# Kernel tuning notes

Measured on AMD Instinct MI355X. Metric: run time of the kernel, lower is better.

The kernel has to match this reference:

```python
import jax, jax.numpy as jnp
import numpy as np

# Model dims (from CerebroOriginal defaults)
B, C, T, E, H, NB, NC = 256, 14, 8, 180, 5, 6, 4
DH = E // H          # 36
S = C * T            # 112 tokens
MLP = 4 * E          # 720


def qdq(x):
    """Int8 per-tensor fake quant-dequant (Brevitas Int8ActPerTensorFloat-style), STE."""
    s = jnp.maximum(jnp.max(jnp.abs(x)) / 127.0, 1e-8)
    y = jnp.clip(jnp.round(x / s), -128.0, 127.0) * s
    return x + jax.lax.stop_gradient(y - x)


def ln(x, g, b):
    m = jnp.mean(x, axis=-1, keepdims=True)
    v = jnp.var(x, axis=-1, keepdims=True)
    return (x - m) * jax.lax.rsqrt(v + 1e-5) * g + b


def qlinear(x, w, b):
    """QuantLinear: int8 input quant + int8 per-tensor weight quant, float bias."""
    return qdq(x) @ qdq(w).T + b


def setup_inputs() -> dict:
    key = jax.random.key(0)
    ks = jax.random.split(key, 16)
    r = lambda k, sh: (0.05 * jax.random.normal(k, sh)).astype(jnp.float32)
    f32 = jnp.float32
    return {
        "x": jax.random.normal(ks[0], (B, C, T), dtype=f32),
        "proj_w": r(ks[1], (E, C)), "proj_b": jnp.zeros((E,), f32),
        "ln1_g": jnp.ones((NB, E), f32), "ln1_b": jnp.zeros((NB, E), f32),
        "wq": r(ks[2], (NB, E, E)), "bq": jnp.zeros((NB, E), f32),
        "wk": r(ks[3], (NB, E, E)), "bk": jnp.zeros((NB, E), f32),
        "wv": r(ks[4], (NB, E, E)), "bv": jnp.zeros((NB, E), f32),
        "wo": r(ks[5], (NB, E, E)), "bo": jnp.zeros((NB, E), f32),
        "ln2_g": jnp.ones((NB, E), f32), "ln2_b": jnp.zeros((NB, E), f32),
        "fc1_w": r(ks[6], (NB, MLP, E)), "fc1_b": jnp.zeros((NB, MLP), f32),
        "fc2_w": r(ks[7], (NB, E, MLP)), "fc2_b": jnp.zeros((NB, E), f32),
        "fn_g": jnp.ones((E,), f32), "fn_b": jnp.zeros((E,), f32),
        "cls_w": r(ks[8], (NC, E)), "cls_b": jnp.zeros((NC,), f32),
    }


def forward(x, proj_w, proj_b, ln1_g, ln1_b, wq, bq, wk, bk, wv, bv, wo, bo,
            ln2_g, ln2_b, fc1_w, fc1_b, fc2_w, fc2_b, fn_g, fn_b, cls_w, cls_b):
    # input quant -> [B,T,C] -> proj -> [B,T,E]
    h = jnp.transpose(qdq(x), (0, 2, 1))
    h = qlinear(h, proj_w, proj_b)
    # expand over channels then flatten to [B, C*T, E] (channel-major token layout)
    h = jnp.broadcast_to(h[:, None], (B, C, T, E)).reshape(B, S, E)

    for i in range(NB):
        # --- attention sub-block ---
        r1 = h
        a = qdq(ln(h, ln1_g[i], ln1_b[i])).reshape(B, C, T, E)
        if i % 2 == 0:  # temporal attention: attend over T within each channel
            a = a.reshape(B * C, T, E)
            L = T
        else:           # channel attention: attend over C within each time step
            a = jnp.transpose(a, (0, 2, 1, 3)).reshape(B * T, C, E)
            L = C
        q = qlinear(a, wq[i], bq[i]).reshape(-1, L, H, DH)
        k = qlinear(a, wk[i], bk[i]).reshape(-1, L, H, DH)
        v = qlinear(a, wv[i], bv[i]).reshape(-1, L, H, DH)
        scores = jnp.einsum('nlhd,nmhd->nhlm', q, k) / jnp.sqrt(jnp.float32(DH))
        att = jax.nn.softmax(scores, axis=-1)
        o = jnp.einsum('nhlm,nmhd->nlhd', att, v).reshape(-1, L, E)
        o = qlinear(o, wo[i], bo[i])
        if i % 2 == 0:
            o = o.reshape(B, C, T, E)
        else:
            o = jnp.transpose(o.reshape(B, T, C, E), (0, 2, 1, 3))
        h = r1 + o.reshape(B, S, E)

        # --- MLP sub-block ---
        r2 = h
        m = qdq(ln(h, ln2_g[i], ln2_b[i]))
        m = qlinear(m, fc1_w[i], fc1_b[i])
        m = qdq(jax.nn.gelu(m))
        m = qlinear(m, fc2_w[i], fc2_b[i])
        h = r2 + m

    h = qdq(ln(h, fn_g, fn_b))
    pooled = jnp.mean(h, axis=1)                 # QuantMean over tokens -> [B, E]
    return qlinear(pooled, cls_w, cls_b)         # [B, NC]


def reference(x, proj_w, proj_b, ln1_g, ln1_b, wq, bq, wk, bk, wv, bv, wo, bo,
              ln2_g, ln2_b, fc1_w, fc1_b, fc2_w, fc2_b, fn_g, fn_b, cls_w, cls_b):
    return forward(x, proj_w, proj_b, ln1_g, ln1_b, wq, bq, wk, bk, wv, bv, wo, bo,
                   ln2_g, ln2_b, fc1_w, fc1_b, fc2_w, fc2_b, fn_g, fn_b, cls_w, cls_b)
```

## Files before the change

### kernel.cpp

```cpp
#include <hip/hip_runtime.h>
#include <math.h>

#define E 180
#define S 112
#define Bb 256
#define CC 14
#define TT 8
#define HH 5
#define DH 36
#define NBLK 6
#define MLPD 720
#define M_TOK (Bb*S)
#define BUF ((size_t)M_TOK * E)

#define KP1 192
#define KP2 736

#define WQ8_OFF   0
#define WK8_OFF   36864
#define WV8_OFF   73728
#define WO8_OFF   110592
#define FC18_OFF  147456
#define FC28_OFF  285696
#define WBLK      427008

#define SLOT_X    0
#define SLOT_PW   1
#define SLOT_CW   2
#define SLOT_POOL 3
#define SLOT_FLN  4
#define SLOT_WQ   8
#define SLOT_WK   16
#define SLOT_WV   24
#define SLOT_WO   32
#define SLOT_FC1  40
#define SLOT_FC2  48
#define SLOT_LN1  56
#define SLOT_O    64
#define SLOT_LN2  72
#define SLOT_GELU 80
#define SLOT_GXMAX 88
#define SLOT_GXA   96
#define SLOT_GXB   104
#define SLOT_GDIR  112

#define XL (-0.7535)
#define XR (-0.7515)

typedef unsigned long long ull;
typedef __attribute__((ext_vector_type(8))) short short8;
typedef __attribute__((ext_vector_type(4))) float f32x4;

__device__ __forceinline__ double slot_scale(const ull* s){
  return fmax(__longlong_as_double((long long)*s) / 127.0, 1e-8);
}
__device__ __forceinline__ void atomic_max_d(ull* p, double v){
  atomicMax(p, (ull)__double_as_longlong(v));
}
__device__ __forceinline__ ull enc_d(double d){
  ull b = (ull)__double_as_longlong(d);
  return (b >> 63) ? ~b : (b | 0x8000000000000000ULL);
}
__device__ __forceinline__ double dec_d(ull k){
  ull b = (k >> 63) ? (k ^ 0x8000000000000000ULL) : ~k;
  return __longlong_as_double((long long)b);
}
__device__ __forceinline__ float q_int_d(double x, double s){
  double r = rint(x / s);
  r = fmin(fmax(r, -128.0), 127.0);
  return (float)r;
}
__device__ __forceinline__ float q_int_fast(double x, double s, float sf){
  float t = (float)x / sf;
  float r = rintf(t);
  if(fabsf(t - r) > 0.497f || fabsf(t) > 126.f){
    double rd = rint(x / s);
    rd = fmin(fmax(rd, -128.0), 127.0);
    return (float)rd;
  }
  return r;
}
__device__ __forceinline__ unsigned short f2bf(float f){
  return (unsigned short)(__float_as_uint(f) >> 16);
}
__device__ __forceinline__ double gelu_d(double x){
  double t = tanh(0.7978845608028654*(x + 0.044715*x*x*x));
  return 0.5*x*(1.0 + t);
}
__device__ __forceinline__ float gelu_f(float x){
  float t = tanhf(0.7978845608f*(x + 0.044715f*x*x*x));
  return 0.5f*x*(1.f + t);
}
__device__ __forceinline__ int pmap(int row, int mode){
  if(mode == 0) return row;
  int b = row / S; int r = row - b*S; int t = r / CC; int c = r - t*CC;
  return b*S + c*TT + t;
}
__device__ __forceinline__ int pmap_inv(int row){
  int b = row / S; int r = row - b*S; int c = r / TT; int t = r - c*TT;
  return b*S + t*CC + c;
}

__global__ void init_slots(ull* slots){
  int t = threadIdx.x;
  slots[t] = (t >= SLOT_GXB && t < SLOT_GXB + NBLK) ? ~0ULL : 0ULL;
}

__global__ void amax_f32(const float* __restrict__ src, int seglen, ull* slots){
  int seg = blockIdx.y;
  const float* p = src + (size_t)seg * seglen;
  float m = 0.f;
  for(int i = blockIdx.x*256 + threadIdx.x; i < seglen; i += gridDim.x*256)
    m = fmaxf(m, fabsf(p[i]));
  __shared__ float red[256];
  red[threadIdx.x] = m;
  __syncthreads();
  for(int off = 128; off > 0; off >>= 1){
    if(threadIdx.x < off) red[threadIdx.x] = fmaxf(red[threadIdx.x], red[threadIdx.x+off]);
    __syncthreads();
  }
  if(threadIdx.x == 0) atomic_max_d(slots + seg, (double)red[0]);
}

__global__ void quant_w(const float* __restrict__ src, int N, int K,
                        int Npad, int Kpad, const ull* __restrict__ slotbase,
                        unsigned short* __restrict__ dst, size_t dstoff){
  int i = blockIdx.y;
  int e = blockIdx.x*256 + threadIdx.x;
  int tot = Npad * Kpad;
  if(e >= tot) return;
  int n = e / Kpad, k = e - n*Kpad;
  double s = slot_scale(slotbase + i);
  float val = 0.f;
  if(n < N && k < K)
    val = q_int_d((double)src[(size_t)i*N*K + (size_t)n*K + k], s);
  dst[(size_t)i*WBLK + dstoff + e] = f2bf(val);
}

__global__ void proj_bcast(const float* __restrict__ x, const float* __restrict__ pw,
                           const float* __restrict__ pb, double* __restrict__ h,
                           const ull* __restrict__ sx_slot,
                           const ull* __restrict__ sw_slot){
  int tid = blockIdx.x*256 + threadIdx.x;
  if(tid >= Bb*TT*E) return;
  int e = tid % E; int bt = tid / E; int t = bt % TT; int b = bt / TT;
  double sx = slot_scale(sx_slot), sw = slot_scale(sw_slot);
  float acc = 0.f;
  for(int c = 0; c < CC; c++)
    acc += q_int_d((double)x[(b*CC + c)*TT + t], sx) * q_int_d((double)pw[e*CC + c], sw);
  double o = (double)acc * (sx * sw) + (double)pb[e];
  for(int c = 0; c < CC; c++)
    h[((size_t)b*S + c*TT + t)*E + e] = o;
}

__device__ __forceinline__ void ln_row(const double* __restrict__ in, size_t base, int lane,
    const float* __restrict__ g, const float* __restrict__ bta,
    double& y0, double& y1, double& y2){
  double x0 = in[base + lane];
  double x1 = in[base + lane + 64];
  double x2 = (lane < E - 128) ? in[base + lane + 128] : 0.0;
  double sum = x0 + x1 + x2;
  for(int m = 32; m > 0; m >>= 1) sum += __shfl_xor(sum, m);
  double mean = sum * (1.0 / E);
  double d0 = x0 - mean, d1 = x1 - mean;
  double d2 = (lane < E - 128) ? (x2 - mean) : 0.0;
  double vs = d0*d0 + d1*d1 + d2*d2;
  for(int m = 32; m > 0; m >>= 1) vs += __shfl_xor(vs, m);
  double inv = 1.0 / sqrt(vs * (1.0 / E) + 1e-5);
  y0 = d0*inv*(double)g[lane]      + (double)bta[lane];
  y1 = d1*inv*(double)g[lane+64]   + (double)bta[lane+64];
  y2 = (lane < E - 128) ? (d2*inv*(double)g[lane+128] + (double)bta[lane+128]) : 0.0;
}

template<bool WRITE>
__global__ void __launch_bounds__(256) ln_amax(const double* __restrict__ in,
    double* __restrict__ out, const float* __restrict__ g,
    const float* __restrict__ bta, ull* amax_slot){
  int wave = threadIdx.x >> 6, lane = threadIdx.x & 63;
  double amx = 0.0;
  for(int tok = blockIdx.x*4 + wave; tok < M_TOK; tok += gridDim.x*4){
    size_t base = (size_t)tok * E;
    double y0, y1, y2;
    ln_row(in, base, lane, g, bta, y0, y1, y2);
    if(WRITE){
      out[base + lane]      = y0;
      out[base + lane + 64] = y1;
      if(lane < E - 128) out[base + lane + 128] = y2;
    }
    amx = fmax(amx, fmax(fabs(y0), fabs(y1)));
    if(lane < E - 128) amx = fmax(amx, fabs(y2));
  }
  for(int m = 32; m > 0; m >>= 1) amx = fmax(amx, __shfl_xor(amx, m));
  __shared__ double red[4];
  if(lane == 0) red[wave] = amx;
  __syncthreads();
  if(threadIdx.x == 0){
    double m = fmax(fmax(red[0], red[1]), fmax(red[2], red[3]));
    atomic_max_d(amax_slot, m);
  }
}

template<int PERM>
__global__ void __launch_bounds__(256) ln_quant(const double* __restrict__ in,
    unsigned short* __restrict__ dst, const float* __restrict__ g,
    const float* __restrict__ bta, const ull* __restrict__ slot){
  int wave = threadIdx.x >> 6, lane = threadIdx.x & 63;
  double s = slot_scale(slot); float sf = (float)s;
  for(int tok = blockIdx.x*4 + wave; tok < M_TOK; tok += gridDim.x*4){
    size_t base = (size_t)tok * E;
    double y0, y1, y2;
    ln_row(in, base, lane, g, bta, y0, y1, y2);
    int d = PERM ? pmap_inv(tok) : tok;
    unsigned short* dr = dst + (size_t)d*KP1;
    dr[lane]       = f2bf(q_int_fast(y0, s, sf));
    dr[lane + 64]  = f2bf(q_int_fast(y1, s, sf));
    dr[lane + 128] = (lane < E - 128) ? f2bf(q_int_fast(y2, s, sf)) : (unsigned short)0;
  }
}

__global__ void __launch_bounds__(256) quant_act(const double* __restrict__ src,
                          unsigned short* __restrict__ dst,
                          const ull* __restrict__ slot){
  int tid = blockIdx.x*256 + threadIdx.x;
  if(tid >= M_TOK*KP1/8) return;
  int idx8 = tid*8;
  int row = idx8 / KP1, k0 = idx8 - row*KP1;
  double s = slot_scale(slot); float sf = (float)s;
  const double* sp = src + (size_t)row*E;
  unsigned short v[8];
  #pragma unroll
  for(int j = 0; j < 8; j++){
    int k = k0 + j;
    v[j] = (k < E) ? f2bf(q_int_fast(sp[k], s, sf)) : (unsigned short)0;
  }
  *reinterpret_cast<short8*>(dst + (size_t)row*KP1 + k0) = *reinterpret_cast<short8*>(v);
}

__global__ void __launch_bounds__(256) quant_mid(const float* __restrict__ midacc,
                          unsigned short* __restrict__ dst,
                          const ull* __restrict__ slotA, const ull* __restrict__ slotW,
                          const ull* __restrict__ slotG, const float* __restrict__ bias){
  int tid = blockIdx.x*256 + threadIdx.x;
  if(tid >= M_TOK*KP2/8) return;
  int idx8 = tid*8;
  int row = idx8 / KP2, k0 = idx8 - row*KP2;
  double sAW = slot_scale(slotA) * slot_scale(slotW);
  double sg = slot_scale(slotG);
  float sAWf = (float)sAW, sgf = (float)sg;
  const float* sp = midacc + (size_t)row*MLPD;
  unsigned short v[8];
  #pragma unroll
  for(int j = 0; j < 8; j++){
    int k = k0 + j;
    if(k < MLPD){
      float a = sp[k];
      float y = fmaf(a, sAWf, bias[k]);
      float gf = gelu_f(y);
      float t = gf / sgf;
      float r = rintf(t);
      if(fabsf(t - r) > 0.497f || fabsf(t) > 126.f){
        double outv = (double)a*sAW + (double)bias[k];
        double rd = rint(gelu_d(outv)/sg);
        rd = fmin(fmax(rd, -128.0), 127.0);
        r = (float)rd;
      }
      v[j] = f2bf(r);
    } else v[j] = 0;
  }
  *reinterpret_cast<short8*>(dst + (size_t)row*KP2 + k0) = *reinterpret_cast<short8*>(v);
}

__global__ void gelu_finalize(ull* slots, int i){
  if(threadIdx.x != 0) return;
  double am = 0.0;
  ull kx = slots[SLOT_GXMAX + i];
  if(kx){ double x = dec_d(kx); if(fabs(x) < 1e299) am = fabs(gelu_d(x)); }
  ull ka = slots[SLOT_GXA + i];
  if(ka){ double x = dec_d(ka); if(fabs(x) < 1e299) am = fmax(am, fabs(gelu_d(x))); }
  ull kb = slots[SLOT_GXB + i];
  if(kb != ~0ULL){ double x = dec_d(kb); if(fabs(x) < 1e299) am = fmax(am, fabs(gelu_d(x))); }
  am = fmax(am, __longlong_as_double((long long)slots[SLOT_GDIR + i]));
  slots[SLOT_GELU + i] = (ull)__double_as_longlong(am);
}

__global__ void __launch_bounds__(256) gemm_qkv(
    const unsigned short* __restrict__ A8,
    const unsigned short* __restrict__ Wq, float* __restrict__ outq)
{
  int sel = blockIdx.x;
  const unsigned short* W8 = Wq + (size_t)sel*36864;
  float* outF = outq + (size_t)sel*((size_t)M_TOK*E);
  int wave = threadIdx.x >> 6, lane = threadIdx.x & 63;
  int m0 = blockIdx.y*64 + wave*16;
  int lr = lane & 15, lg = lane >> 4;
  const unsigned short* Arow = A8 + (size_t)(m0 + lr)*KP1 + lg*8;
  const unsigned short* Wbase = W8 + (size_t)lr*KP1 + lg*8;
  f32x4 acc[12];
  #pragma unroll
  for(int j = 0; j < 12; j++) acc[j] = (f32x4){0.f,0.f,0.f,0.f};
  for(int kk = 0; kk < KP1/32; kk++){
    short8 a = *reinterpret_cast<const short8*>(Arow + kk*32);
    const unsigned short* Wp = Wbase + kk*32;
    #pragma unroll
    for(int j = 0; j < 12; j++){
      short8 b = *reinterpret_cast<const short8*>(Wp + (size_t)j*16*KP1);
      acc[j] = __builtin_amdgcn_mfma_f32_16x16x32_bf16(a, b, acc[j], 0, 0, 0);
    }
  }
  #pragma unroll
  for(int j = 0; j < 12; j++){
    int col = j*16 + lr;
    if(col >= E) continue;
    #pragma unroll
    for(int r = 0; r < 4; r++){
      int row = m0 + lg*4 + r;
      outF[(size_t)row*E + col] = acc[j][r];
    }
  }
}

template<int NT, int EPI>
__global__ void __launch_bounds__(256) gemm_mfma(
    const unsigned short* __restrict__ A8, int Kpad,
    const unsigned short* __restrict__ W8,
    const float* __restrict__ bias, int Nreal,
    float* __restrict__ outF, double* __restrict__ outH,
    const ull* __restrict__ slotA, const ull* __restrict__ slotW,
    ull* cand, int permOut,
    const float* __restrict__ lng, const float* __restrict__ lnb)
{
  int wave = threadIdx.x >> 6, lane = threadIdx.x & 63;
  int m0 = blockIdx.y*64 + wave*16;
  int tbase = blockIdx.x*NT;
  int lr = lane & 15, lg = lane >> 4;
  const unsigned short* Arow = A8 + (size_t)(m0 + lr)*Kpad + lg*8;
  const unsigned short* Wbase = W8 + (size_t)(tbase*16 + lr)*Kpad + lg*8;
  f32x4 acc[NT];
  #pragma unroll
  for(int j = 0; j < NT; j++) acc[j] = (f32x4){0.f,0.f,0.f,0.f};
  int ksteps = Kpad >> 5;
  for(int kk = 0; kk < ksteps; kk++){
    short8 a = *reinterpret_cast<const short8*>(Arow + kk*32);
    const unsigned short* Wp = Wbase + kk*32;
    #pragma unroll
    for(int j = 0; j < NT; j++){
      short8 b = *reinterpret_cast<const short8*>(Wp + (size_t)j*16*Kpad);
      acc[j] = __builtin_amdgcn_mfma_f32_16x16x32_bf16(a, b, acc[j], 0, 0, 0);
    }
  }
  double sAW = slot_scale(slotA) * slot_scale(slotW);
  if(EPI == 0){
    #pragma unroll
    for(int j = 0; j < NT; j++){
      int col = (tbase + j)*16 + lr;
      if(col >= Nreal) continue;
      #pragma unroll
      for(int r = 0; r < 4; r++)
        outF[(size_t)(m0 + lg*4 + r)*Nreal + col] = acc[j][r];
    }
  } else if(EPI == 2){
    double xmax = -1e300, xa = -1e300, xb = 1e300, dir = 0.0;
    #pragma unroll
    for(int j = 0; j < NT; j++){
      int col = (tbase + j)*16 + lr;
      if(col >= Nreal) continue;
      #pragma unroll
      for(int r = 0; r < 4; r++){
        int row = m0 + lg*4 + r;
        float a = acc[j][r];
        double outv = (double)a * sAW + (double)bias[col];
        outF[(size_t)row*Nreal + col] = a;
        xmax = fmax(xmax, outv);
        if(outv <= XL) xa = fmax(xa, outv);
        else if(outv < XR) dir = fmax(dir, fabs(gelu_d(outv)));
        if(outv >= XR) xb = fmin(xb, outv);
      }
    }
    for(int m = 32; m > 0; m >>= 1){
      xmax = fmax(xmax, __shfl_xor(xmax, m));
      xa   = fmax(xa,   __shfl_xor(xa,   m));
      xb   = fmin(xb,   __shfl_xor(xb,   m));
      dir  = fmax(dir,  __shfl_xor(dir,  m));
    }
    __shared__ double r0[4], r1[4], r2[4], r3[4];
    if(lane == 0){ r0[wave]=xmax; r1[wave]=xa; r2[wave]=xb; r3[wave]=dir; }
    __syncthreads();
    if(threadIdx.x == 0){
      double M0=r0[0], A0=r1[0], B0=r2[0], D0=r3[0];
      for(int w = 1; w < 4; w++){
        M0 = fmax(M0, r0[w]); A0 = fmax(A0, r1[w]);
        B0 = fmin(B0, r2[w]); D0 = fmax(D0, r3[w]);
      }
      atomicMax(cand + SLOT_GXMAX, enc_d(M0));
      atomicMax(cand + SLOT_GXA,   enc_d(A0));
      atomicMin(cand + SLOT_GXB,   enc_d(B0));
      atomicMax(cand + SLOT_GDIR,  (ull)__double_as_longlong(D0));
    }
  } else {
    double amx = 0.0;
    #pragma unroll
    for(int r = 0; r < 4; r++){
      int row = m0 + lg*4 + r;
      int orow = pmap(row, permOut);
      double hvr[NT];
      double rsum = 0.0;
      #pragma unroll
      for(int j = 0; j < NT; j++){
        int col = j*16 + lr;
        double nh = 0.0;
        if(col < Nreal){
          double outv = (double)acc[j][r] * sAW + (double)bias[col];
          size_t idx = (size_t)orow*E + col;
          nh = outH[idx] + outv;
          outH[idx] = nh;
        }
        hvr[j] = nh;
        rsum += nh;
      }
      for(int m = 1; m <= 8; m <<= 1) rsum += __shfl_xor(rsum, m);
      double mean = rsum * (1.0 / E);
      double vsum = 0.0;
      #pragma unroll
      for(int j = 0; j < NT; j++){
        int col = j*16 + lr;
        double d_ = (col < Nreal) ? (hvr[j] - mean) : 0.0;
        vsum += d_*d_;
      }
      for(int m = 1; m <= 8; m <<= 1) vsum += __shfl_xor(vsum, m);
      double inv = 1.0 / sqrt(vsum * (1.0 / E) + 1e-5);
      #pragma unroll
      for(int j = 0; j < NT; j++){
        int col = j*16 + lr;
        if(col < Nreal){
          double y = (hvr[j] - mean)*inv*(double)lng[col] + (double)lnb[col];
          amx = fmax(amx, fabs(y));
        }
      }
    }
    for(int m = 1; m <= 32; m <<= 1) amx = fmax(amx, __shfl_xor(amx, m));
    __shared__ double redA[4];
    if(lane == 0) redA[wave] = amx;
    __syncthreads();
    if(threadIdx.x == 0)
      atomic_max_d(cand, fmax(fmax(redA[0], redA[1]), fmax(redA[2], redA[3])));
  }
}

template<int L>
__global__ void __launch_bounds__(64) attn_v2(const float* __restrict__ qa,
    const float* __restrict__ ka, const float* __restrict__ va,
    double* __restrict__ o,
    const float* __restrict__ bq, const float* __restrict__ bk,
    const float* __restrict__ bv,
    const ull* __restrict__ sLN, const ull* __restrict__ sWq,
    const ull* __restrict__ sWk, const ull* __restrict__ sWv,
    ull* amax_slot){
  const int LP = L + 1;
  __shared__ float qs[L*DH], kT[DH*L], vs[L*DH];
  __shared__ double att[L*LP];
  __shared__ double QB[L], KB[L], BBs;
  int tid = threadIdx.x;
  double sA = slot_scale(sLN);
  double dq = sA * slot_scale(sWq);
  double dk = sA * slot_scale(sWk);
  double dv = sA * slot_scale(sWv);
  double dqk = dq * dk;
  double am = 0.0;
  for(int gseg = 0; gseg < 4; gseg++){
    int segid = blockIdx.x*4 + gseg;
    int n = segid / HH, hh = segid % HH;
    size_t rowbase = (size_t)n*L*E + hh*DH;
    const float* bqh = bq + hh*DH;
    const float* bkh = bk + hh*DH;
    const float* bvh = bv + hh*DH;
    for(int idx = tid; idx < L*DH; idx += 64){
      int l = idx / DH, d = idx - l*DH;
      size_t g = rowbase + (size_t)l*E + d;
      float qv = qa[g], kv = ka[g], vv = va[g];
      qs[l*DH+d] = qv;
      kT[d*L+l]  = kv;
      vs[l*DH+d] = vv;
    }
    __syncthreads();
    if(tid < L){
      double s = 0.0;
      for(int d = 0; d < DH; d++) s += (double)qs[tid*DH+d] * (double)bkh[d];
      QB[tid] = s;
    } else if(tid >= 16 && tid < 16 + L){
      int m = tid - 16;
      double s = 0.0;
      for(int d = 0; d < DH; d++) s += (double)kT[d*L+m] * (double)bqh[d];
      KB[m] = s;
    } else if(tid == 63){
      double s = 0.0;
      for(int d = 0; d < DH; d++) s += (double)bqh[d] * (double)bkh[d];
      BBs = s;
    }
    __syncthreads();
    for(int idx = tid; idx < L*L; idx += 64){
      int l = idx / L, m = idx - l*L;
      double si = 0.0;
      for(int d = 0; d < DH; d++) si += (double)qs[l*DH+d] * (double)kT[d*L+m];
      att[l*LP+m] = (dqk*si + dq*QB[l] + dk*KB[m] + BBs) * (1.0 / 6.0);
    }
    __syncthreads();
    if(tid < L){
      double mx = -1e300;
      for(int m = 0; m < L; m++) mx = fmax(mx, att[tid*LP+m]);
      double sm = 0.0;
      for(int m = 0; m < L; m++){ double e_ = exp(att[tid*LP+m] - mx); att[tid*LP+m] = e_; sm += e_; }
      double r = 1.0 / sm;
      for(int m = 0; m < L; m++) att[tid*LP+m] *= r;
    }
    __syncthreads();
    for(int idx = tid; idx < L*DH; idx += 64){
      int l = idx / DH, d = idx - l*DH;
      double bvd = (double)bvh[d];
      double s = 0.0;
      for(int m = 0; m < L; m++) s += att[l*LP+m] * ((double)vs[m*DH+d]*dv + bvd);
      o[rowbase + (size_t)l*E + d] = s;
      am = fmax(am, fabs(s));
    }
    __syncthreads();
  }
  for(int m = 32; m > 0; m >>= 1) am = fmax(am, __shfl_xor(am, m));
  if(tid == 0) atomic_max_d(amax_slot, am);
}

__global__ void __launch_bounds__(256) pooled_kernel(const double* __restrict__ lnout,
    double* __restrict__ pooled, const ull* __restrict__ slot_ln,
    ull* slot_pooled){
  int tid = blockIdx.x*256 + threadIdx.x;
  double am = 0.0;
  if(tid < Bb*E){
    int b = tid / E, e = tid - (tid/E)*E;
    double sl = slot_scale(slot_ln); float slf = (float)sl;
    double sum = 0.0;
    for(int s = 0; s < S; s++)
      sum += (double)q_int_fast(lnout[((size_t)b*S + s)*E + e], sl, slf) * sl;
    double pv = sum * (1.0 / S);
    pooled[(size_t)b*E + e] = pv;
    am = fabs(pv);
  }
  for(int m = 32; m > 0; m >>= 1) am = fmax(am, __shfl_xor(am, m));
  if((threadIdx.x & 63) == 0) atomic_max_d(slot_pooled, am);
}

__global__ void __launch_bounds__(64) cls_kernel(const double* __restrict__ pooled,
    const float* __restrict__ cw, const float* __restrict__ cb,
    float* __restrict__ out, const ull* __restrict__ sp,
    const ull* __restrict__ sw){
  int tid = blockIdx.x*64 + threadIdx.x;
  if(tid >= Bb*4) return;
  int b = tid >> 2, j = tid & 3;
  double s1 = slot_scale(sp), s2 = slot_scale(sw);
  float acc = 0.f;
  for(int e = 0; e < E; e++)
    acc += q_int_d(pooled[b*E + e], s1) * q_int_d((double)cw[j*E + e], s2);
  out[tid] = (float)((double)acc * (s1 * s2) + (double)cb[j]);
}

extern "C" void kernel_launch(void* const* d_in, const int* in_sizes, int n_in,
                              void* d_out, int out_size, void* d_ws, size_t ws_size,
                              hipStream_t stream){
  const float* x      = (const float*)d_in[0];
  const float* proj_w = (const float*)d_in[1];
  const float* proj_b = (const float*)d_in[2];
  const float* ln1_g  = (const float*)d_in[3];
  const float* ln1_b  = (const float*)d_in[4];
  const float* wq     = (const float*)d_in[5];
  const float* bq     = (const float*)d_in[6];
  const float* wk     = (const float*)d_in[7];
  const float* bk     = (const float*)d_in[8];
  const float* wv     = (const float*)d_in[9];
  const float* bv     = (const float*)d_in[10];
  const float* wo     = (const float*)d_in[11];
  const float* bo     = (const float*)d_in[12];
  const float* ln2_g  = (const float*)d_in[13];
  const float* ln2_b  = (const float*)d_in[14];
  const float* fc1_w  = (const float*)d_in[15];
  const float* fc1_b  = (const float*)d_in[16];
  const float* fc2_w  = (const float*)d_in[17];
  const float* fc2_b  = (const float*)d_in[18];
  const float* fn_g   = (const float*)d_in[19];
  const float* fn_b   = (const float*)d_in[20];
  const float* cls_w  = (const float*)d_in[21];
  const float* cls_b  = (const float*)d_in[22];
  float* outp = (float*)d_out;

  char* base = (char*)d_ws;
  ull*    slots  = (ull*)base;
  double* h      = (double*)(base + 4096);
  double* scr    = h + BUF;
  float*  facc   = (float*)(scr + BUF);
  float*  qacc   = facc;
  float*  midacc = facc;
  double* pooled = (double*)facc;
  unsigned short* act8 = (unsigned short*)(facc + (size_t)M_TOK*MLPD);
  unsigned short* mid8 = act8 + (size_t)M_TOK*KP1;
  unsigned short* w8   = mid8 + (size_t)M_TOK*KP2;

  init_slots<<<1, 128, 0, stream>>>(slots);

  amax_f32<<<dim3(32,1), 256, 0, stream>>>(x,      Bb*CC*TT, slots + SLOT_X);
  amax_f32<<<dim3(1,1),  256, 0, stream>>>(proj_w, E*CC,     slots + SLOT_PW);
  amax_f32<<<dim3(1,1),  256, 0, stream>>>(cls_w,  4*E,      slots + SLOT_CW);
  amax_f32<<<dim3(4,NBLK),  256, 0, stream>>>(wq,    E*E,    slots + SLOT_WQ);
  amax_f32<<<dim3(4,NBLK),  256, 0, stream>>>(wk,    E*E,    slots + SLOT_WK);
  amax_f32<<<dim3(4,NBLK),  256, 0, stream>>>(wv,    E*E,    slots + SLOT_WV);
  amax_f32<<<dim3(4,NBLK),  256, 0, stream>>>(wo,    E*E,    slots + SLOT_WO);
  amax_f32<<<dim3(16,NBLK), 256, 0, stream>>>(fc1_w, MLPD*E, slots + SLOT_FC1);
  amax_f32<<<dim3(16,NBLK), 256, 0, stream>>>(fc2_w, MLPD*E, slots + SLOT_FC2);

  quant_w<<<dim3((KP1*KP1+255)/256, NBLK), 256, 0, stream>>>(wq, E, E, KP1, KP1, slots+SLOT_WQ, w8, WQ8_OFF);
  quant_w<<<dim3((KP1*KP1+255)/256, NBLK), 256, 0, stream>>>(wk, E, E, KP1, KP1, slots+SLOT_WK, w8, WK8_OFF);
  quant_w<<<dim3((KP1*KP1+255)/256, NBLK), 256, 0, stream>>>(wv, E, E, KP1, KP1, slots+SLOT_WV, w8, WV8_OFF);
  quant_w<<<dim3((KP1*KP1+255)/256, NBLK), 256, 0, stream>>>(wo, E, E, KP1, KP1, slots+SLOT_WO, w8, WO8_OFF);
  quant_w<<<dim3((MLPD*KP1+255)/256, NBLK), 256, 0, stream>>>(fc1_w, MLPD, E, MLPD, KP1, slots+SLOT_FC1, w8, FC18_OFF);
  quant_w<<<dim3((KP1*KP2+255)/256, NBLK), 256, 0, stream>>>(fc2_w, E, MLPD, KP1, KP2, slots+SLOT_FC2, w8, FC28_OFF);

  proj_bcast<<<(Bb*TT*E + 255)/256, 256, 0, stream>>>(x, proj_w, proj_b, h,
                                                      slots + SLOT_X, slots + SLOT_PW);

  const int QA_GRID = (M_TOK*KP1/8 + 255)/256;
  const int QM_GRID = (M_TOK*KP2/8 + 255)/256;
  const int LN_GRID = 1792;

  ln_amax<false><<<LN_GRID, 256, 0, stream>>>(h, nullptr, ln1_g, ln1_b, slots + SLOT_LN1);

  for(int i = 0; i < NBLK; i++){
    int pi = i & 1;
    const unsigned short* wb = w8 + (size_t)i*WBLK;
    if(pi == 0)
      ln_quant<0><<<LN_GRID, 256, 0, stream>>>(h, act8, ln1_g + i*E, ln1_b + i*E, slots + SLOT_LN1 + i);
    else
      ln_quant<1><<<LN_GRID, 256, 0, stream>>>(h, act8, ln1_g + i*E, ln1_b + i*E, slots + SLOT_LN1 + i);
    gemm_qkv<<<dim3(3, M_TOK/64), 256, 0, stream>>>(act8, wb + WQ8_OFF, qacc);
    if(pi == 0){
      int nseg = (M_TOK/TT)*HH;
      attn_v2<TT><<<nseg/4, 64, 0, stream>>>(qacc, qacc + (size_t)M_TOK*E, qacc + (size_t)2*M_TOK*E, scr,
          bq + i*E, bk + i*E, bv + i*E,
          slots+SLOT_LN1+i, slots+SLOT_WQ+i, slots+SLOT_WK+i, slots+SLOT_WV+i,
          slots + SLOT_O + i);
    } else {
      int nseg = (M_TOK/CC)*HH;
      attn_v2<CC><<<nseg/4, 64, 0, stream>>>(qacc, qacc + (size_t)M_TOK*E, qacc + (size_t)2*M_TOK*E, scr,
          bq + i*E, bk + i*E, bv + i*E,
          slots+SLOT_LN1+i, slots+SLOT_WQ+i, slots+SLOT_WK+i, slots+SLOT_WV+i,
          slots + SLOT_O + i);
    }
    quant_act<<<QA_GRID, 256, 0, stream>>>(scr, act8, slots + SLOT_O + i);
    gemm_mfma<12,3><<<dim3(1, M_TOK/64), 256, 0, stream>>>(act8, KP1, wb + WO8_OFF, bo + i*E, E,
        nullptr, h, slots+SLOT_O+i, slots+SLOT_WO+i, slots+SLOT_LN2+i, pi,
        ln2_g + i*E, ln2_b + i*E);
    ln_quant<0><<<LN_GRID, 256, 0, stream>>>(h, act8, ln2_g + i*E, ln2_b + i*E, slots + SLOT_LN2 + i);
    gemm_mfma<9,2><<<dim3(5, M_TOK/64), 256, 0, stream>>>(act8, KP1, wb + FC18_OFF, fc1_b + i*MLPD, MLPD,
        midacc, nullptr, slots+SLOT_LN2+i, slots+SLOT_FC1+i, slots + i, 0, nullptr, nullptr);
    gelu_finalize<<<1, 64, 0, stream>>>(slots, i);
    quant_mid<<<QM_GRID, 256, 0, stream>>>(midacc, mid8,
        slots+SLOT_LN2+i, slots+SLOT_FC1+i, slots+SLOT_GELU+i, fc1_b + i*MLPD);
    ull* nslot = (i < 5) ? (slots + SLOT_LN1 + i + 1) : (slots + SLOT_FLN);
    const float* ng = (i < 5) ? (ln1_g + (i+1)*E) : fn_g;
    const float* nb = (i < 5) ? (ln1_b + (i+1)*E) : fn_b;
    gemm_mfma<12,3><<<dim3(1, M_TOK/64), 256, 0, stream>>>(mid8, KP2, wb + FC28_OFF, fc2_b + i*E, E,
        nullptr, h, slots+SLOT_GELU+i, slots+SLOT_FC2+i, nslot, 0, ng, nb);
  }

  ln_amax<true><<<LN_GRID, 256, 0, stream>>>(h, scr, fn_g, fn_b, slots + SLOT_FLN);
  pooled_kernel<<<(Bb*E + 255)/256, 256, 0, stream>>>(scr, pooled, slots + SLOT_FLN, slots + SLOT_POOL);
  cls_kernel<<<(Bb*4 + 63)/64, 64, 0, stream>>>(pooled, cls_w, cls_b, outp,
                                                slots + SLOT_POOL, slots + SLOT_CW);
}
```

Before: 3.634 ms.

## Recompute fc1 GEMM with fused GELU-quant epilogue instead of storing fp32 accumulators

The fc1 GEMM's first pass now only gathers GELU amax statistics and no longer writes the fp32 M×720 accumulator. A second fc1 GEMM pass with a new epilogue applies bias, GELU and int8 quantisation and writes bf16 into mid8 directly, replacing the separate quant_mid kernel. The pad columns are zeroed once up front. The fp32 write and re-read traffic is traded for running the fc1 GEMM twice. Separately, the residual gemm now prefetches the h values before the K loop to hide load latency.

```diff
diff --git a/kernel.cpp b/kernel.cpp
--- a/kernel.cpp
+++ b/kernel.cpp
@@ -106,6 +106,14 @@
   slots[t] = (t >= SLOT_GXB && t < SLOT_GXB + NBLK) ? ~0ULL : 0ULL;
 }
 
+__global__ void zero_pad(unsigned short* __restrict__ mid8){
+  int tid = blockIdx.x*256 + threadIdx.x;
+  if(tid >= M_TOK*2) return;
+  int row = tid >> 1, half = tid & 1;
+  short8 z = (short8){0,0,0,0,0,0,0,0};
+  *reinterpret_cast<short8*>(mid8 + (size_t)row*KP2 + MLPD + half*8) = z;
+}
+
 __global__ void amax_f32(const float* __restrict__ src, int seglen, ull* slots){
   int seg = blockIdx.y;
   const float* p = src + (size_t)seg * seglen;
@@ -234,40 +242,6 @@
     v[j] = (k < E) ? f2bf(q_int_fast(sp[k], s, sf)) : (unsigned short)0;
   }
   *reinterpret_cast<short8*>(dst + (size_t)row*KP1 + k0) = *reinterpret_cast<short8*>(v);
-}
-
-__global__ void __launch_bounds__(256) quant_mid(const float* __restrict__ midacc,
-                          unsigned short* __restrict__ dst,
-                          const ull* __restrict__ slotA, const ull* __restrict__ slotW,
-                          const ull* __restrict__ slotG, const float* __restrict__ bias){
-  int tid = blockIdx.x*256 + threadIdx.x;
-  if(tid >= M_TOK*KP2/8) return;
-  int idx8 = tid*8;
-  int row = idx8 / KP2, k0 = idx8 - row*KP2;
-  double sAW = slot_scale(slotA) * slot_scale(slotW);
-  double sg = slot_scale(slotG);
-  float sAWf = (float)sAW, sgf = (float)sg;
-  const float* sp = midacc + (size_t)row*MLPD;
-  unsigned short v[8];
-  #pragma unroll
-  for(int j = 0; j < 8; j++){
-    int k = k0 + j;
-    if(k < MLPD){
-      float a = sp[k];
-      float y = fmaf(a, sAWf, bias[k]);
-      float gf = gelu_f(y);
-      float t = gf / sgf;
-      float r = rintf(t);
-      if(fabsf(t - r) > 0.497f || fabsf(t) > 126.f){
-        double outv = (double)a*sAW + (double)bias[k];
-        double rd = rint(gelu_d(outv)/sg);
-        rd = fmin(fmax(rd, -128.0), 127.0);
-        r = (float)rd;
-      }
-      v[j] = f2bf(r);
-    } else v[j] = 0;
-  }
-  *reinterpret_cast<short8*>(dst + (size_t)row*KP2 + k0) = *reinterpret_cast<short8*>(v);
 }
 
 __global__ void gelu_finalize(ull* slots, int i){
@@ -324,8 +298,9 @@
     const unsigned short* __restrict__ A8, int Kpad,
     const unsigned short* __restrict__ W8,
     const float* __restrict__ bias, int Nreal,
-    float* __restrict__ outF, double* __restrict__ outH,
+    double* __restrict__ outH, unsigned short* __restrict__ outU16,
     const ull* __restrict__ slotA, const ull* __restrict__ slotW,
+    const ull* __restrict__ slotG,
     ull* cand, int permOut,
     const float* __restrict__ lng, const float* __restrict__ lnb)
 {
@@ -335,6 +310,22 @@
   int lr = lane & 15, lg = lane >> 4;
   const unsigned short* Arow = A8 + (size_t)(m0 + lr)*Kpad + lg*8;
   const unsigned short* Wbase = W8 + (size_t)(tbase*16 + lr)*Kpad + lg*8;
+
+  double hv[EPI == 3 ? 4 : 1][EPI == 3 ? NT : 1];
+  int orow_r[EPI == 3 ? 4 : 1];
+  if(EPI == 3){
+    #pragma unroll
+    for(int r = 0; r < 4; r++){
+      int row = m0 + lg*4 + r;
+      orow_r[r] = pmap(row, permOut);
+      #pragma unroll
+      for(int j = 0; j < NT; j++){
+        int col = j*16 + lr;
+        hv[r][j] = (col < Nreal) ? outH[(size_t)orow_r[r]*E + col] : 0.0;
+      }
+    }
+  }
+
   f32x4 acc[NT];
   #pragma unroll
   for(int j = 0; j < NT; j++) acc[j] = (f32x4){0.f,0.f,0.f,0.f};
@@ -349,16 +340,8 @@
     }
   }
   double sAW = slot_scale(slotA) * slot_scale(slotW);
-  if(EPI == 0){
-    #pragma unroll
-    for(int j = 0; j < NT; j++){
-      int col = (tbase + j)*16 + lr;
-      if(col >= Nreal) continue;
-      #pragma unroll
-      for(int r = 0; r < 4; r++)
-        outF[(size_t)(m0 + lg*4 + r)*Nreal + col] = acc[j][r];
-    }
-  } else if(EPI == 2){
+
+  if(EPI == 2){
     double xmax = -1e300, xa = -1e300, xb = 1e300, dir = 0.0;
     #pragma unroll
     for(int j = 0; j < NT; j++){
@@ -366,10 +349,7 @@
       if(col >= Nreal) continue;
       #pragma unroll
       for(int r = 0; r < 4; r++){
-        int row = m0 + lg*4 + r;
-        float a = acc[j][r];
-        double outv = (double)a * sAW + (double)bias[col];
-        outF[(size_t)row*Nreal + col] = a;
+        double outv = (double)acc[j][r] * sAW + (double)bias[col];
         xmax = fmax(xmax, outv);
         if(outv <= XL) xa = fmax(xa, outv);
         else if(outv < XR) dir = fmax(dir, fabs(gelu_d(outv)));
@@ -396,12 +376,35 @@
       atomicMin(cand + SLOT_GXB,   enc_d(B0));
       atomicMax(cand + SLOT_GDIR,  (ull)__double_as_longlong(D0));
     }
+  } else if(EPI == 4){
+    double sg = slot_scale(slotG);
+    float sAWf = (float)sAW, sgf = (float)sg;
+    #pragma unroll
+    for(int j = 0; j < NT; j++){
+      int col = (tbase + j)*16 + lr;
+      if(col >= Nreal) continue;
+      #pragma unroll
+      for(int r = 0; r < 4; r++){
+        int row = m0 + lg*4 + r;
+        float a = acc[j][r];
+        float y = fmaf(a, sAWf, bias[col]);
+        float gf = gelu_f(y);
+        float t = gf / sgf;
+        float rq = rintf(t);
+        if(fabsf(t - rq) > 0.497f || fabsf(t) > 126.f){
+          double outv = (double)a*sAW + (double)bias[col];
+          double rd = rint(gelu_d(outv)/sg);
+          rd = fmin(fmax(rd, -128.0), 127.0);
+          rq = (float)rd;
+        }
+        outU16[(size_t)row*KP2 + col] = f2bf(rq);
+      }
+    }
   } else {
     double amx = 0.0;
     #pragma unroll
     for(int r = 0; r < 4; r++){
-      int row = m0 + lg*4 + r;
-      int orow = pmap(row, permOut);
+      int orow = orow_r[r];
       double hvr[NT];
       double rsum = 0.0;
       #pragma unroll
@@ -410,9 +413,8 @@
         double nh = 0.0;
         if(col < Nreal){
           double outv = (double)acc[j][r] * sAW + (double)bias[col];
-          size_t idx = (size_t)orow*E + col;
-          nh = outH[idx] + outv;
-          outH[idx] = nh;
+          nh = hv[r][j] + outv;
+          outH[(size_t)orow*E + col] = nh;
         }
         hvr[j] = nh;
         rsum += nh;
@@ -432,8 +434,8 @@
       for(int j = 0; j < NT; j++){
         int col = j*16 + lr;
         if(col < Nreal){
-          double y = (hvr[j] - mean)*inv*(double)lng[col] + (double)lnb[col];
-          amx = fmax(amx, fabs(y));
+          double yy = (hvr[j] - mean)*inv*(double)lng[col] + (double)lnb[col];
+          amx = fmax(amx, fabs(yy));
         }
       }
     }
@@ -476,10 +478,9 @@
     for(int idx = tid; idx < L*DH; idx += 64){
       int l = idx / DH, d = idx - l*DH;
       size_t g = rowbase + (size_t)l*E + d;
-      float qv = qa[g], kv = ka[g], vv = va[g];
-      qs[l*DH+d] = qv;
-      kT[d*L+l]  = kv;
-      vs[l*DH+d] = vv;
+      qs[l*DH+d] = qa[g];
+      kT[d*L+l]  = ka[g];
+      vs[l*DH+d] = va[g];
     }
     __syncthreads();
     if(tid < L){
@@ -594,13 +595,13 @@
   double* scr    = h + BUF;
   float*  facc   = (float*)(scr + BUF);
   float*  qacc   = facc;
-  float*  midacc = facc;
   double* pooled = (double*)facc;
   unsigned short* act8 = (unsigned short*)(facc + (size_t)M_TOK*MLPD);
   unsigned short* mid8 = act8 + (size_t)M_TOK*KP1;
   unsigned short* w8   = mid8 + (size_t)M_TOK*KP2;
 
   init_slots<<<1, 128, 0, stream>>>(slots);
+  zero_pad<<<(M_TOK*2 + 255)/256, 256, 0, stream>>>(mid8);
 
   amax_f32<<<dim3(32,1), 256, 0, stream>>>(x,      Bb*CC*TT, slots + SLOT_X);
   amax_f32<<<dim3(1,1),  256, 0, stream>>>(proj_w, E*CC,     slots + SLOT_PW);
@@ -623,7 +624,6 @@
                                                       slots + SLOT_X, slots + SLOT_PW);
 
   const int QA_GRID = (M_TOK*KP1/8 + 255)/256;
-  const int QM_GRID = (M_TOK*KP2/8 + 255)/256;
   const int LN_GRID = 1792;
 
   ln_amax<false><<<LN_GRID, 256, 0, stream>>>(h, nullptr, ln1_g, ln1_b, slots + SLOT_LN1);
@@ -651,19 +651,19 @@
     }
     quant_act<<<QA_GRID, 256, 0, stream>>>(scr, act8, slots + SLOT_O + i);
     gemm_mfma<12,3><<<dim3(1, M_TOK/64), 256, 0, stream>>>(act8, KP1, wb + WO8_OFF, bo + i*E, E,
-        nullptr, h, slots+SLOT_O+i, slots+SLOT_WO+i, slots+SLOT_LN2+i, pi,
+        h, nullptr, slots+SLOT_O+i, slots+SLOT_WO+i, nullptr, slots+SLOT_LN2+i, pi,
         ln2_g + i*E, ln2_b + i*E);
     ln_quant<0><<<LN_GRID, 256, 0, stream>>>(h, act8, ln2_g + i*E, ln2_b + i*E, slots + SLOT_LN2 + i);
     gemm_mfma<9,2><<<dim3(5, M_TOK/64), 256, 0, stream>>>(act8, KP1, wb + FC18_OFF, fc1_b + i*MLPD, MLPD,
-        midacc, nullptr, slots+SLOT_LN2+i, slots+SLOT_FC1+i, slots + i, 0, nullptr, nullptr);
+        nullptr, nullptr, slots+SLOT_LN2+i, slots+SLOT_FC1+i, nullptr, slots + i, 0, nullptr, nullptr);
     gelu_finalize<<<1, 64, 0, stream>>>(slots, i);
-    quant_mid<<<QM_GRID, 256, 0, stream>>>(midacc, mid8,
-        slots+SLOT_LN2+i, slots+SLOT_FC1+i, slots+SLOT_GELU+i, fc1_b + i*MLPD);
+    gemm_mfma<9,4><<<dim3(5, M_TOK/64), 256, 0, stream>>>(act8, KP1, wb + FC18_OFF, fc1_b + i*MLPD, MLPD,
+        nullptr, mid8, slots+SLOT_LN2+i, slots+SLOT_FC1+i, slots+SLOT_GELU+i, nullptr, 0, nullptr, nullptr);
     ull* nslot = (i < 5) ? (slots + SLOT_LN1 + i + 1) : (slots + SLOT_FLN);
     const float* ng = (i < 5) ? (ln1_g + (i+1)*E) : fn_g;
     const float* nb = (i < 5) ? (ln1_b + (i+1)*E) : fn_b;
     gemm_mfma<12,3><<<dim3(1, M_TOK/64), 256, 0, stream>>>(mid8, KP2, wb + FC28_OFF, fc2_b + i*E, E,
-        nullptr, h, slots+SLOT_GELU+i, slots+SLOT_FC2+i, nslot, 0, ng, nb);
+        h, nullptr, slots+SLOT_GELU+i, slots+SLOT_FC2+i, nullptr, nslot, 0, ng, nb);
   }
 
   ln_amax<true><<<LN_GRID, 256, 0, stream>>>(h, scr, fn_g, fn_b, slots + SLOT_FLN);
```

New measurement: 3.447 ms. -5.1%, faster.
